# Kernel optimization log

Measured on AMD Instinct MI355X. Metric: run time of the kernel, lower is better.

The kernel has to match this reference:

```python
import jax, jax.numpy as jnp
import numpy as np

S, N, M = 8, 4096, 64          # snapshots, atoms, total neighbors (sum of max_num_neighs)
L = 20.0                        # periodic box length
R_CS, R_C = 2.0, 6.0            # smooth cutoff radii
DSUB = 16                       # dim_sub_net
PAD_FRAC = 0.15                 # fraction of -1 padded neighbor slots


def _mlp(x, params):
    # DenseChainNet: Linear -> relu between layers, no activation after last layer
    n = len(params)
    for i, (W, b) in enumerate(params):
        x = x @ W + b
        if i < n - 1:
            x = jax.nn.relu(x)
    return x


def _lin(k, fan_in, fan_out):
    k1, k2 = jax.random.split(k)
    s = 1.0 / np.sqrt(fan_in)
    W = jax.random.uniform(k1, (fan_in, fan_out), minval=-s, maxval=s, dtype=jnp.float32)
    b = jax.random.uniform(k2, (fan_out,), minval=-s, maxval=s, dtype=jnp.float32)
    return W, b


def setup_inputs() -> dict:
    key = jax.random.key(0)
    ks = jax.random.split(key, 12)
    inputs = jax.random.uniform(ks[0], (S, N, 3), dtype=jnp.float32) * L
    input_types = jax.random.randint(ks[1], (S, N), 0, 2)
    # neighbor indices, guaranteed != self, with -1 padding
    base = jnp.arange(N, dtype=jnp.int32)[None, :, None]
    off = jax.random.randint(ks[2], (S, N, M), 1, N)
    neigh = (base + off) % N
    pad = jax.random.uniform(ks[3], (S, N, M)) < PAD_FRAC
    neigh_list = jnp.where(pad, -1, neigh).astype(jnp.int32)
    es1_w, es1_b = _lin(ks[4], 2, 4)
    es2_w, es2_b = _lin(ks[5], 4, 4)
    fs1_w, fs1_b = _lin(ks[6], 4, 4)
    fs2_w, fs2_b = _lin(ks[7], 4, 4)
    en1_w, en1_b = _lin(ks[8], 4, 8)
    en2_w, en2_b = _lin(ks[9], 8, 16)
    en3_w, en3_b = _lin(ks[10], 16, 32)
    return dict(inputs=inputs, input_types=input_types, neigh_list=neigh_list,
                es1_w=es1_w, es1_b=es1_b, es2_w=es2_w, es2_b=es2_b,
                fs1_w=fs1_w, fs1_b=fs1_b, fs2_w=fs2_w, fs2_b=fs2_b,
                en1_w=en1_w, en1_b=en1_b, en2_w=en2_w, en2_b=en2_b,
                en3_w=en3_w, en3_b=en3_b)


def reference(inputs, input_types, neigh_list,
              es1_w, es1_b, es2_w, es2_b,
              fs1_w, fs1_b, fs2_w, fs2_b,
              en1_w, en1_b, en2_w, en2_b, en3_w, en3_b):
    mask = neigh_list == -1                               # [S,N,M]
    idx = jnp.where(mask, 0, neigh_list)
    flat = idx.reshape(S, N * M)
    # gather neighbor coordinates with periodic minimum-image convention
    pos_j = jnp.take_along_axis(inputs, flat[..., None], axis=1).reshape(S, N, M, 3)
    d = pos_j - inputs[:, :, None, :]
    d = d - L * jnp.round(d / L)
    r = jnp.sqrt(jnp.sum(d * d, axis=-1) + 1e-12)         # [S,N,M]
    # smooth cutoff: s(r) = 1/r for r<r_cs, cosine switch to 0 at r_c
    u = (r - R_CS) / (R_C - R_CS)
    sw = jnp.where(r < R_CS, 1.0,
                   jnp.where(r < R_C, 0.5 * jnp.cos(jnp.pi * u) + 0.5, 0.0))
    s_ij = jnp.where(mask, 0.0, sw / r)                   # [S,N,M]
    r_ij = d * (s_ij / r)[..., None]                      # s(r) * d / r, [S,N,M,3]
    # species pair descriptor (symmetrized over pair order)
    neigh_types = jnp.take_along_axis(input_types, flat, axis=1).reshape(S, N, M)
    self_t = jnp.broadcast_to(input_types[:, :, None], (S, N, M))
    pairs = jnp.stack([self_t, neigh_types], axis=-1).astype(jnp.float32).reshape(-1, 2)
    es = [(es1_w, es1_b), (es2_w, es2_b)]
    td = _mlp(pairs, es) + _mlp(pairs[:, ::-1], es)
    td = _mlp(td, [(fs1_w, fs1_b), (fs2_w, fs2_b)]).reshape(S, N, M, -1)  # [S,N,M,4]
    s_tilde = (td * s_ij[..., None]).reshape(S * N * M, -1)
    G = _mlp(s_tilde, [(en1_w, en1_b), (en2_w, en2_b), (en3_w, en3_b)]).reshape(S, N, M, -1)  # [S,N,M,32]
    r_tilde = jnp.concatenate([s_ij[..., None], r_ij], axis=-1)            # [S,N,M,4]
    R = jnp.einsum('snmd,snmk->sndk', r_tilde, G[..., :DSUB])              # [S,N,4,16]
    R1 = jnp.einsum('snmd,sndk->snmk', r_tilde, R)                         # [S,N,M,16]
    D = jnp.einsum('snmg,snmk->sngk', G, R1)                               # [S,N,32,16]
    return D
```

## Files before the change

kernel.cpp:

```cpp
#include <hip/hip_runtime.h>
#include <math.h>

#define SS 8
#define NN 4096
#define MM 64
#define LBOX 20.0f

__global__ __launch_bounds__(256) void desc_kernel(
    const float* __restrict__ pos,
    const int*   __restrict__ types,
    const int*   __restrict__ neigh,
    const float* __restrict__ es1_w, const float* __restrict__ es1_b,
    const float* __restrict__ es2_w, const float* __restrict__ es2_b,
    const float* __restrict__ fs1_w, const float* __restrict__ fs1_b,
    const float* __restrict__ fs2_w, const float* __restrict__ fs2_b,
    const float* __restrict__ en1_w, const float* __restrict__ en1_b,
    const float* __restrict__ en2_w, const float* __restrict__ en2_b,
    const float* __restrict__ en3_w, const float* __restrict__ en3_b,
    float* __restrict__ out)
{
    __shared__ alignas(16) float sh_vt[32];
    __shared__ alignas(16) float sh_b1[8];
    __shared__ alignas(16) float sh_W2t[128];
    __shared__ alignas(16) float sh_b2[16];
    __shared__ alignas(16) float sh_W3[512];
    __shared__ alignas(16) float sh_b3[32];
    __shared__ alignas(16) float sh_h2[4][64*17];
    __shared__ alignas(16) float sh_rt[4][64*5];
    __shared__ alignas(16) float sh_P[4][64];
    __shared__ alignas(16) float sh_A[4][128];

    const int tid = threadIdx.x;

    if (tid < 4) {
        const float ti = (float)(tid >> 1), tj = (float)(tid & 1);
        float e[4] = {0.f, 0.f, 0.f, 0.f};
        #pragma unroll
        for (int swp = 0; swp < 2; ++swp) {
            const float a = swp ? tj : ti, b = swp ? ti : tj;
            float h[4];
            #pragma unroll
            for (int k = 0; k < 4; ++k)
                h[k] = fmaxf(a * es1_w[k] + b * es1_w[4 + k] + es1_b[k], 0.f);
            #pragma unroll
            for (int k = 0; k < 4; ++k) {
                float acc = es2_b[k];
                #pragma unroll
                for (int j = 0; j < 4; ++j) acc += h[j] * es2_w[j * 4 + k];
                e[k] += acc;
            }
        }
        float f[4];
        #pragma unroll
        for (int k = 0; k < 4; ++k) {
            float acc = fs1_b[k];
            #pragma unroll
            for (int j = 0; j < 4; ++j) acc += e[j] * fs1_w[j * 4 + k];
            f[k] = fmaxf(acc, 0.f);
        }
        float td[4];
        #pragma unroll
        for (int k = 0; k < 4; ++k) {
            float acc = fs2_b[k];
            #pragma unroll
            for (int j = 0; j < 4; ++j) acc += f[j] * fs2_w[j * 4 + k];
            td[k] = acc;
        }
        #pragma unroll
        for (int o = 0; o < 8; ++o) {
            float acc = 0.f;
            #pragma unroll
            for (int d = 0; d < 4; ++d) acc += td[d] * en1_w[d * 8 + o];
            sh_vt[tid * 8 + o] = acc;
        }
    }
    if (tid < 8)  sh_b1[tid] = en1_b[tid];
    if (tid < 16) sh_b2[tid] = en2_b[tid];
    if (tid < 32) sh_b3[tid] = en3_b[tid];
    if (tid < 128) { const int k = tid >> 3, i = tid & 7; sh_W2t[tid] = en2_w[i * 16 + k]; }
    sh_W3[tid]       = en3_w[tid];
    sh_W3[tid + 256] = en3_w[tid + 256];
    __syncthreads();

    const int wave = tid >> 6;
    const int lane = tid & 63;
    const int atom = blockIdx.x * 4 + wave;
    const int sbase = atom & ~(NN - 1);

    float* __restrict__ h2w = sh_h2[wave];
    float* __restrict__ rtw = sh_rt[wave];

    const float xi = pos[atom * 3 + 0];
    const float yi = pos[atom * 3 + 1];
    const float zi = pos[atom * 3 + 2];
    const int   ti = types[atom];

    const int nb  = neigh[atom * MM + lane];
    const int msk = nb < 0;
    const int j   = msk ? 0 : nb;
    const int gj  = sbase + j;

    float dx = pos[gj * 3 + 0] - xi;
    float dy = pos[gj * 3 + 1] - yi;
    float dz = pos[gj * 3 + 2] - zi;
    dx -= LBOX * rintf(dx * (1.0f / LBOX));
    dy -= LBOX * rintf(dy * (1.0f / LBOX));
    dz -= LBOX * rintf(dz * (1.0f / LBOX));
    const float r2   = fmaf(dx, dx, fmaf(dy, dy, fmaf(dz, dz, 1e-12f)));
    const float rinv = rsqrtf(r2);
    const float r    = r2 * rinv;
    const float u    = (r - 2.0f) * 0.25f;
    float swv = 0.5f * __cosf(3.14159265358979323846f * u) + 0.5f;
    swv = (r < 2.0f) ? 1.0f : ((r < 6.0f) ? swv : 0.0f);
    const float sij   = msk ? 0.0f : swv * rinv;
    const float scale = sij * rinv;
    const float rt0 = sij, rt1 = dx * scale, rt2 = dy * scale, rt3 = dz * scale;

    const int tj = types[gj];
    const int tt = ti * 2 + tj;

    float h1[8];
    {
        const float4 va = *(const float4*)(sh_vt + tt * 8);
        const float4 vb = *(const float4*)(sh_vt + tt * 8 + 4);
        h1[0] = fmaxf(fmaf(sij, va.x, sh_b1[0]), 0.f);
        h1[1] = fmaxf(fmaf(sij, va.y, sh_b1[1]), 0.f);
        h1[2] = fmaxf(fmaf(sij, va.z, sh_b1[2]), 0.f);
        h1[3] = fmaxf(fmaf(sij, va.w, sh_b1[3]), 0.f);
        h1[4] = fmaxf(fmaf(sij, vb.x, sh_b1[4]), 0.f);
        h1[5] = fmaxf(fmaf(sij, vb.y, sh_b1[5]), 0.f);
        h1[6] = fmaxf(fmaf(sij, vb.z, sh_b1[6]), 0.f);
        h1[7] = fmaxf(fmaf(sij, vb.w, sh_b1[7]), 0.f);
    }

    #pragma unroll 4
    for (int k = 0; k < 16; ++k) {
        const float4 wa = *(const float4*)(sh_W2t + k * 8);
        const float4 wb = *(const float4*)(sh_W2t + k * 8 + 4);
        float acc = sh_b2[k];
        acc = fmaf(h1[0], wa.x, acc); acc = fmaf(h1[1], wa.y, acc);
        acc = fmaf(h1[2], wa.z, acc); acc = fmaf(h1[3], wa.w, acc);
        acc = fmaf(h1[4], wb.x, acc); acc = fmaf(h1[5], wb.y, acc);
        acc = fmaf(h1[6], wb.z, acc); acc = fmaf(h1[7], wb.w, acc);
        h2w[lane * 17 + k] = fmaxf(acc, 0.f);
    }
    rtw[lane * 5 + 0] = rt0;
    rtw[lane * 5 + 1] = rt1;
    rtw[lane * 5 + 2] = rt2;
    rtw[lane * 5 + 3] = rt3;
    __syncthreads();

    const int hh = lane >> 2, dd = lane & 3;
    float pe = 0.f, q = 0.f;
    #pragma unroll 16
    for (int m = 0; m < 64; ++m) {
        const float hv = h2w[m * 17 + hh];
        const float rv = rtw[m * 5 + dd];
        pe = fmaf(hv, rv, pe);
        q += rv;
    }
    sh_P[wave][lane] = pe;
    __syncthreads();

    {
        const int g0 = hh, g1 = hh + 16;
        float a0 = sh_b3[g0] * q;
        float a1 = sh_b3[g1] * q;
        #pragma unroll 8
        for (int h = 0; h < 16; ++h) {
            const float pv = sh_P[wave][h * 4 + dd];
            a0 = fmaf(sh_W3[h * 32 + g0], pv, a0);
            a1 = fmaf(sh_W3[h * 32 + g1], pv, a1);
        }
        sh_A[wave][lane]      = a0;
        sh_A[wave][lane + 64] = a1;
    }
    __syncthreads();

    {
        const int g = lane >> 1, koff = (lane & 1) * 8;
        const float4 Ag = *(const float4*)&sh_A[wave][g * 4];
        float o[8];
        #pragma unroll
        for (int jj = 0; jj < 8; ++jj) {
            const float4 Ak = *(const float4*)&sh_A[wave][(koff + jj) * 4];
            o[jj] = fmaf(Ag.x, Ak.x, fmaf(Ag.y, Ak.y, fmaf(Ag.z, Ak.z, Ag.w * Ak.w)));
        }
        float* op = out + (size_t)atom * 512 + lane * 8;
        *(float4*)(op)     = make_float4(o[0], o[1], o[2], o[3]);
        *(float4*)(op + 4) = make_float4(o[4], o[5], o[6], o[7]);
    }
}

extern "C" void kernel_launch(void* const* d_in, const int* in_sizes, int n_in,
                              void* d_out, int out_size, void* d_ws, size_t ws_size,
                              hipStream_t stream) {
    const float* pos   = (const float*)d_in[0];
    const int*   typ   = (const int*)d_in[1];
    const int*   ngh   = (const int*)d_in[2];
    desc_kernel<<<dim3((SS * NN) / 4), dim3(256), 0, stream>>>(
        pos, typ, ngh,
        (const float*)d_in[3],  (const float*)d_in[4],
        (const float*)d_in[5],  (const float*)d_in[6],
        (const float*)d_in[7],  (const float*)d_in[8],
        (const float*)d_in[9],  (const float*)d_in[10],
        (const float*)d_in[11], (const float*)d_in[12],
        (const float*)d_in[13], (const float*)d_in[14],
        (const float*)d_in[15], (const float*)d_in[16],
        (float*)d_out);
}
```

Baseline: 151.9 us.

## Use bf16 MFMA for the neighbor contraction and restructure shared-memory layouts

Replaces the scalar 64-neighbor reduction of h2 against r_tilde with bf16 MFMA 16x16x32 instructions, using a ones-vector MFMA to get the column sums. Stores h2 and r_tilde as bf16 in transposed LDS layouts and transposes W3 for vectorized loads in the next stage. Layer-2 weights and biases are now read directly from global memory rather than staged in LDS. The aim is to cut LDS traffic and VALU work in the reduction, at the cost of bf16 precision loss in the descriptor.

Result: faster. 130.5 us (-14.0%).

```diff
diff --git a/kernel.cpp b/kernel.cpp
--- a/kernel.cpp
+++ b/kernel.cpp
@@ -5,6 +5,15 @@
 #define NN 4096
 #define MM 64
 #define LBOX 20.0f
+
+typedef __attribute__((ext_vector_type(8))) short short8;
+typedef __attribute__((ext_vector_type(4))) float floatx4;
+
+__device__ inline unsigned short f2bf(float x) {
+    unsigned u = __float_as_uint(x);
+    u += 0x7fffu + ((u >> 16) & 1u);
+    return (unsigned short)(u >> 16);
+}
 
 __global__ __launch_bounds__(256) void desc_kernel(
     const float* __restrict__ pos,
@@ -19,16 +28,13 @@
     const float* __restrict__ en3_w, const float* __restrict__ en3_b,
     float* __restrict__ out)
 {
-    __shared__ alignas(16) float sh_vt[32];
-    __shared__ alignas(16) float sh_b1[8];
-    __shared__ alignas(16) float sh_W2t[128];
-    __shared__ alignas(16) float sh_b2[16];
-    __shared__ alignas(16) float sh_W3[512];
-    __shared__ alignas(16) float sh_b3[32];
-    __shared__ alignas(16) float sh_h2[4][64*17];
-    __shared__ alignas(16) float sh_rt[4][64*5];
-    __shared__ alignas(16) float sh_P[4][64];
+    __shared__ alignas(16) unsigned short sh_h2[4][16][72];
+    __shared__ alignas(16) unsigned short sh_rt[4][4][72];
+    __shared__ alignas(16) float sh_PT[4][4][20];
+    __shared__ alignas(16) float sh_W3t[32][20];
     __shared__ alignas(16) float sh_A[4][128];
+    __shared__ alignas(16) float sh_vt[4][8];
+    __shared__ float sh_b3[32];
 
     const int tid = threadIdx.x;
 
@@ -71,24 +77,22 @@
             float acc = 0.f;
             #pragma unroll
             for (int d = 0; d < 4; ++d) acc += td[d] * en1_w[d * 8 + o];
-            sh_vt[tid * 8 + o] = acc;
-        }
-    }
-    if (tid < 8)  sh_b1[tid] = en1_b[tid];
-    if (tid < 16) sh_b2[tid] = en2_b[tid];
+            sh_vt[tid][o] = acc;
+        }
+    }
+    {
+        int i = tid;
+        sh_W3t[i & 31][i >> 5] = en3_w[i];
+        i += 256;
+        sh_W3t[i & 31][i >> 5] = en3_w[i];
+    }
     if (tid < 32) sh_b3[tid] = en3_b[tid];
-    if (tid < 128) { const int k = tid >> 3, i = tid & 7; sh_W2t[tid] = en2_w[i * 16 + k]; }
-    sh_W3[tid]       = en3_w[tid];
-    sh_W3[tid + 256] = en3_w[tid + 256];
     __syncthreads();
 
     const int wave = tid >> 6;
     const int lane = tid & 63;
     const int atom = blockIdx.x * 4 + wave;
     const int sbase = atom & ~(NN - 1);
-
-    float* __restrict__ h2w = sh_h2[wave];
-    float* __restrict__ rtw = sh_rt[wave];
 
     const float xi = pos[atom * 3 + 0];
     const float yi = pos[atom * 3 + 1];
@@ -114,63 +118,67 @@
     swv = (r < 2.0f) ? 1.0f : ((r < 6.0f) ? swv : 0.0f);
     const float sij   = msk ? 0.0f : swv * rinv;
     const float scale = sij * rinv;
-    const float rt0 = sij, rt1 = dx * scale, rt2 = dy * scale, rt3 = dz * scale;
 
     const int tj = types[gj];
     const int tt = ti * 2 + tj;
 
     float h1[8];
     {
-        const float4 va = *(const float4*)(sh_vt + tt * 8);
-        const float4 vb = *(const float4*)(sh_vt + tt * 8 + 4);
-        h1[0] = fmaxf(fmaf(sij, va.x, sh_b1[0]), 0.f);
-        h1[1] = fmaxf(fmaf(sij, va.y, sh_b1[1]), 0.f);
-        h1[2] = fmaxf(fmaf(sij, va.z, sh_b1[2]), 0.f);
-        h1[3] = fmaxf(fmaf(sij, va.w, sh_b1[3]), 0.f);
-        h1[4] = fmaxf(fmaf(sij, vb.x, sh_b1[4]), 0.f);
-        h1[5] = fmaxf(fmaf(sij, vb.y, sh_b1[5]), 0.f);
-        h1[6] = fmaxf(fmaf(sij, vb.z, sh_b1[6]), 0.f);
-        h1[7] = fmaxf(fmaf(sij, vb.w, sh_b1[7]), 0.f);
-    }
-
-    #pragma unroll 4
+        const float4 va = *(const float4*)(&sh_vt[tt][0]);
+        const float4 vb = *(const float4*)(&sh_vt[tt][4]);
+        h1[0] = fmaxf(fmaf(sij, va.x, en1_b[0]), 0.f);
+        h1[1] = fmaxf(fmaf(sij, va.y, en1_b[1]), 0.f);
+        h1[2] = fmaxf(fmaf(sij, va.z, en1_b[2]), 0.f);
+        h1[3] = fmaxf(fmaf(sij, va.w, en1_b[3]), 0.f);
+        h1[4] = fmaxf(fmaf(sij, vb.x, en1_b[4]), 0.f);
+        h1[5] = fmaxf(fmaf(sij, vb.y, en1_b[5]), 0.f);
+        h1[6] = fmaxf(fmaf(sij, vb.z, en1_b[6]), 0.f);
+        h1[7] = fmaxf(fmaf(sij, vb.w, en1_b[7]), 0.f);
+    }
+
+    #pragma unroll
     for (int k = 0; k < 16; ++k) {
-        const float4 wa = *(const float4*)(sh_W2t + k * 8);
-        const float4 wb = *(const float4*)(sh_W2t + k * 8 + 4);
-        float acc = sh_b2[k];
-        acc = fmaf(h1[0], wa.x, acc); acc = fmaf(h1[1], wa.y, acc);
-        acc = fmaf(h1[2], wa.z, acc); acc = fmaf(h1[3], wa.w, acc);
-        acc = fmaf(h1[4], wb.x, acc); acc = fmaf(h1[5], wb.y, acc);
-        acc = fmaf(h1[6], wb.z, acc); acc = fmaf(h1[7], wb.w, acc);
-        h2w[lane * 17 + k] = fmaxf(acc, 0.f);
-    }
-    rtw[lane * 5 + 0] = rt0;
-    rtw[lane * 5 + 1] = rt1;
-    rtw[lane * 5 + 2] = rt2;
-    rtw[lane * 5 + 3] = rt3;
-    __syncthreads();
-
-    const int hh = lane >> 2, dd = lane & 3;
-    float pe = 0.f, q = 0.f;
-    #pragma unroll 16
-    for (int m = 0; m < 64; ++m) {
-        const float hv = h2w[m * 17 + hh];
-        const float rv = rtw[m * 5 + dd];
-        pe = fmaf(hv, rv, pe);
-        q += rv;
-    }
-    sh_P[wave][lane] = pe;
-    __syncthreads();
-
-    {
-        const int g0 = hh, g1 = hh + 16;
-        float a0 = sh_b3[g0] * q;
-        float a1 = sh_b3[g1] * q;
-        #pragma unroll 8
-        for (int h = 0; h < 16; ++h) {
-            const float pv = sh_P[wave][h * 4 + dd];
-            a0 = fmaf(sh_W3[h * 32 + g0], pv, a0);
-            a1 = fmaf(sh_W3[h * 32 + g1], pv, a1);
+        float acc = en2_b[k];
+        #pragma unroll
+        for (int i = 0; i < 8; ++i) acc = fmaf(h1[i], en2_w[i * 16 + k], acc);
+        sh_h2[wave][k][lane] = f2bf(fmaxf(acc, 0.f));
+    }
+    sh_rt[wave][0][lane] = f2bf(sij);
+    sh_rt[wave][1][lane] = f2bf(dx * scale);
+    sh_rt[wave][2][lane] = f2bf(dy * scale);
+    sh_rt[wave][3][lane] = f2bf(dz * scale);
+    __syncthreads();
+
+    const int col = lane & 15;
+    const int q4  = lane >> 4;
+    const int m0  = q4 * 8;
+    floatx4 cP = {0.f, 0.f, 0.f, 0.f};
+    floatx4 cQ = {0.f, 0.f, 0.f, 0.f};
+    const short8 ones = (short8)(short)0x3F80;
+    #pragma unroll
+    for (int ck = 0; ck < 2; ++ck) {
+        const short8 af = *(const short8*)&sh_h2[wave][col][ck * 32 + m0];
+        const short8 bf = *(const short8*)&sh_rt[wave][col & 3][ck * 32 + m0];
+        cP = __builtin_amdgcn_mfma_f32_16x16x32_bf16(af, bf, cP, 0, 0, 0);
+        cQ = __builtin_amdgcn_mfma_f32_16x16x32_bf16(ones, bf, cQ, 0, 0, 0);
+    }
+    if (col < 4) *(floatx4*)&sh_PT[wave][col][q4 * 4] = cP;
+    const float qd = cQ[0];
+    __syncthreads();
+
+    {
+        const int g0 = lane >> 2, dd = lane & 3, g1 = g0 + 16;
+        float a0 = sh_b3[g0] * qd;
+        float a1 = sh_b3[g1] * qd;
+        #pragma unroll
+        for (int c = 0; c < 4; ++c) {
+            const floatx4 pv = *(const floatx4*)&sh_PT[wave][dd][c * 4];
+            const floatx4 w0 = *(const floatx4*)&sh_W3t[g0][c * 4];
+            const floatx4 w1 = *(const floatx4*)&sh_W3t[g1][c * 4];
+            a0 = fmaf(pv.x, w0.x, a0); a0 = fmaf(pv.y, w0.y, a0);
+            a0 = fmaf(pv.z, w0.z, a0); a0 = fmaf(pv.w, w0.w, a0);
+            a1 = fmaf(pv.x, w1.x, a1); a1 = fmaf(pv.y, w1.y, a1);
+            a1 = fmaf(pv.z, w1.z, a1); a1 = fmaf(pv.w, w1.w, a1);
         }
         sh_A[wave][lane]      = a0;
         sh_A[wave][lane + 64] = a1;
```
